# Kernel tuning notes

Hardware: AMD Instinct MI355X
Metric: run time of the kernel (lower is better)

Reference implementation:

```python
import jax, jax.numpy as jnp
import numpy as np

EPS = 1e-8

def l2norm(x, axis):
    # matches torch: x / (sqrt(sum(x^2)) + eps)
    return x / (jnp.sqrt(jnp.sum(x * x, axis=axis, keepdims=True)) + EPS)

def setup_inputs() -> dict:
    key = jax.random.key(0)
    kq, kc, kwq, kbq, kwk, kbk = jax.random.split(key, 6)
    B, QL, SL, D = 128, 512, 1024, 1024
    query = jax.random.normal(kq, (B, QL, D), dtype=jnp.float32)
    context = jax.random.normal(kc, (B, SL, D), dtype=jnp.float32)
    s = 1.0 / np.sqrt(D)
    Wq = jax.random.uniform(kwq, (D, D), jnp.float32, -s, s)
    bq = jax.random.uniform(kbq, (D,), jnp.float32, -s, s)
    Wk = jax.random.uniform(kwk, (D, D), jnp.float32, -s, s)
    bk = jax.random.uniform(kbk, (D,), jnp.float32, -s, s)
    return {"query": query, "context": context, "Wq": Wq, "bq": bq,
            "Wk": Wk, "bk": bk, "smooth": 9.0}

def reference(query, context, Wq, bq, Wk, bk, smooth):
    # linear projections (nn.Linear: x @ W^T + b)
    sim_k = jnp.einsum('bsd,ed->bse', context, Wk) + bk   # (B, SL, D)
    sim_q = jnp.einsum('bqd,ed->bqe', query, Wq) + bq     # (B, QL, D)
    # scores: bmm(sim_k, sim_q^T) -> (B, SL, QL)
    attn = jnp.einsum('bse,bqe->bsq', sim_k, sim_q)
    attn = jnp.where(attn >= 0, attn, 0.1 * attn)          # LeakyReLU(0.1)
    attn = l2norm(attn, axis=2)                            # over queryL dim
    # transpose -> (B, QL, SL), scale, softmax over sourceL
    attn = jax.nn.softmax(attn.transpose(0, 2, 1) * smooth, axis=2)
    # weighted sum of raw context (sim_v = context; fcv unused in original)
    wc = jnp.einsum('bqs,bsd->bqd', attn, context)         # (B, QL, D)
    return l2norm(wc, axis=-1)
```

## Files before the change

### kernel.cpp

```cpp
#include <hip/hip_runtime.h>
#include <hip/hip_bf16.h>

typedef __attribute__((ext_vector_type(8))) short bf16x8;
typedef __attribute__((ext_vector_type(4))) float f32x4;
typedef __attribute__((ext_vector_type(4))) unsigned short u16x4;
typedef __attribute__((ext_vector_type(8))) unsigned short u16x8;

#define DEVINL static __device__ __forceinline__

DEVINL unsigned short f2bf(float f) {
  union { float f; unsigned u; } a; a.f = f;
  return (unsigned short)((a.u + 0x7fffu + ((a.u >> 16) & 1u)) >> 16);
}
DEVINL float bf2f(unsigned short s) {
  union { unsigned u; float f; } a; a.u = ((unsigned)s) << 16; return a.f;
}

typedef __attribute__((address_space(1))) const unsigned char ga_u8;
typedef __attribute__((address_space(3))) unsigned char ls_u8;

constexpr int KD = 1024;
constexpr int NKT = KD / 64;


#define STAGE(b_, mat_, kt_) do { \
    const unsigned short* src_ = (mat_) == 0 ? Az : Bz; \
    const int br_ = (mat_) == 0 ? m0 : n0; \
    char* dst_ = lds + (b_) * 65536 + (mat_) * 32768; \
    _Pragma("unroll") \
    for (int i_ = 0; i_ < 4; ++i_) { \
      const unsigned short* g_ = src_ + (size_t)(br_ + i_ * 64 + sr) * KD + (kt_) * 64 + gc * 8; \
      __builtin_amdgcn_global_load_lds((ga_u8*)g_, (ls_u8*)(dst_ + (i_ * 512 + wv * 64) * 16), 16, 0, 0); \
    } \
  } while (0)

#define KSUB(b_, ks_, STG) do { \
    const char* pA_ = lds + (b_) * 65536; \
    const char* pB_ = pA_ + 32768; \
    const int co_ = (((ks_) * 4 + kg) ^ (ml & 7)) << 4; \
    bf16x8 af_[8], bf_[4]; \
    _Pragma("unroll") \
    for (int mi = 0; mi < 8; ++mi) \
      af_[mi] = *(const bf16x8*)(pA_ + (wm * 128 + mi * 16 + ml) * 128 + co_); \
    _Pragma("unroll") \
    for (int ni = 0; ni < 4; ++ni) \
      bf_[ni] = *(const bf16x8*)(pB_ + (wn * 64 + ni * 16 + ml) * 128 + co_); \
    STG; \
    __builtin_amdgcn_s_setprio(1); \
    _Pragma("unroll") \
    for (int mi = 0; mi < 8; ++mi) \
    _Pragma("unroll") \
    for (int ni = 0; ni < 4; ++ni) \
      acc[mi][ni] = __builtin_amdgcn_mfma_f32_16x16x32_bf16(af_[mi], bf_[ni], acc[mi][ni], 0, 0, 0); \
    __builtin_amdgcn_s_setprio(0); \
  } while (0)

template<int MODE>
__global__ __launch_bounds__(512, 2) void gemm8(
    const unsigned short* __restrict__ A, const unsigned short* __restrict__ B,
    const float* __restrict__ bias, void* __restrict__ Cv,
    float* __restrict__ rnorm2, int mtiles,
    long long sAz, long long sBz, long long sCz, long long sRz, long long sBiasz)
{
  alignas(16) __shared__ char lds[131072];

  const int tid = threadIdx.x;
  const int lane = tid & 63;
  const int wv = tid >> 6;
  const int wm = wv >> 2;
  const int wn = wv & 3;
  const int kg = lane >> 4;
  const int ml = lane & 15;

  const int nwg = (int)gridDim.x;
  const int bid = (int)blockIdx.x;
  const int w = (bid & 7) * (nwg >> 3) + (bid >> 3);
  const int bpz = mtiles * 4;
  const int z = w / bpz;
  const int rem = w - z * bpz;
  const int mt = rem >> 2, nt = rem & 3;
  const int m0 = mt * 256, n0 = nt * 256;

  const unsigned short* Az = A + (size_t)z * (size_t)sAz;
  const unsigned short* Bz = B + (size_t)z * (size_t)sBz;

  const int sr = tid >> 3;
  const int gc = (tid & 7) ^ (sr & 7);

  f32x4 acc[8][4];
  const f32x4 zero4 = {0.f, 0.f, 0.f, 0.f};
#pragma unroll
  for (int i = 0; i < 8; ++i)
#pragma unroll
    for (int j = 0; j < 4; ++j) acc[i][j] = zero4;

  STAGE(0, 0, 0);
  STAGE(0, 1, 0);
  asm volatile("s_waitcnt vmcnt(0)" ::: "memory");
  __builtin_amdgcn_s_barrier();

  for (int t = 0; t < NKT; ++t) {
    const int cur = t & 1;
    const int nxt = cur ^ 1;
    if (t + 1 < NKT) {
      KSUB(cur, 0, STAGE(nxt, 0, t + 1));
      KSUB(cur, 1, STAGE(nxt, 1, t + 1));
    } else {
      KSUB(cur, 0, );
      KSUB(cur, 1, );
    }
    asm volatile("s_waitcnt vmcnt(0)" ::: "memory");
    __builtin_amdgcn_s_barrier();
  }

  float* ew = (float*)(lds + wv * 4352);
  const int erow = lane >> 3;
  const int ec8 = (lane & 7) * 8;
  const int ncol0 = n0 + wn * 64;

  if (MODE == 1) {
    const float* cb = bias + (size_t)z * (size_t)sBiasz;
    f32x4 cb4[8];
#pragma unroll
    for (int mi = 0; mi < 8; ++mi)
      cb4[mi] = *(const f32x4*)(cb + m0 + wm * 128 + mi * 16 + kg * 4);
    float* rn = rnorm2 + (size_t)z * (size_t)sRz;
#pragma unroll
    for (int ni = 0; ni < 4; ++ni) {
      float cs = 0.f;
#pragma unroll
      for (int mi = 0; mi < 8; ++mi)
#pragma unroll
        for (int j = 0; j < 4; ++j) {
          float v = acc[mi][ni][j] + cb4[mi][j];
          v = v >= 0.f ? v : 0.1f * v;
          acc[mi][ni][j] = v;
          cs += v * v;
        }
      cs += __shfl_xor(cs, 16);
      cs += __shfl_xor(cs, 32);
      if (kg == 0) atomicAdd(&rn[ncol0 + ni * 16 + ml], cs);
    }
  }

  f32x4 bv0 = zero4, bv1 = zero4;
  if (MODE == 0) {
    bv0 = *(const f32x4*)(bias + ncol0 + ec8);
    bv1 = *(const f32x4*)(bias + ncol0 + ec8 + 4);
  }

#pragma unroll
  for (int mi = 0; mi < 8; ++mi) {
#pragma unroll
    for (int ni = 0; ni < 4; ++ni)
#pragma unroll
      for (int j = 0; j < 4; ++j)
        ew[(kg * 4 + j) * 68 + ni * 16 + ml] = acc[mi][ni][j];
    const int rb = m0 + wm * 128 + mi * 16;
#pragma unroll
    for (int i = 0; i < 2; ++i) {
      const int r = erow + 8 * i;
      f32x4 x = *(const f32x4*)(&ew[r * 68 + ec8]);
      f32x4 y = *(const f32x4*)(&ew[r * 68 + ec8 + 4]);
      if (MODE == 0 || MODE == 3) {
        unsigned short* C = (unsigned short*)Cv + (size_t)z * (size_t)sCz;
        union { unsigned short s[8]; u16x8 v; } u;
        u.s[0]=f2bf(x[0]+bv0[0]); u.s[1]=f2bf(x[1]+bv0[1]);
        u.s[2]=f2bf(x[2]+bv0[2]); u.s[3]=f2bf(x[3]+bv0[3]);
        u.s[4]=f2bf(y[0]+bv1[0]); u.s[5]=f2bf(y[1]+bv1[1]);
        u.s[6]=f2bf(y[2]+bv1[2]); u.s[7]=f2bf(y[3]+bv1[3]);
        *(u16x8*)(C + (size_t)(rb + r) * 1024 + ncol0 + ec8) = u.v;
      } else {
        float* C = (float*)Cv + (size_t)z * (size_t)sCz;
        *(f32x4*)(C + (size_t)(rb + r) * 1024 + ncol0 + ec8) = x;
        *(f32x4*)(C + (size_t)(rb + r) * 1024 + ncol0 + ec8 + 4) = y;
      }
    }
  }
}

__global__ __launch_bounds__(256) void cvt_bf16_k(
    const float* __restrict__ src, unsigned short* __restrict__ dst)
{
  size_t i = ((size_t)blockIdx.x * 256 + threadIdx.x) * 8;
  f32x4 x = *(const f32x4*)(src + i);
  f32x4 y = *(const f32x4*)(src + i + 4);
  union { unsigned short s[8]; u16x8 v; } u;
  u.s[0]=f2bf(x[0]); u.s[1]=f2bf(x[1]); u.s[2]=f2bf(x[2]); u.s[3]=f2bf(x[3]);
  u.s[4]=f2bf(y[0]); u.s[5]=f2bf(y[1]); u.s[6]=f2bf(y[2]); u.s[7]=f2bf(y[3]);
  *(u16x8*)(dst + i) = u.v;
}

__global__ __launch_bounds__(256) void wT_k(
    const float* __restrict__ W, unsigned short* __restrict__ WT)
{
  __shared__ float tile[32][36];
  const int t = threadIdx.x;
  const int e0 = blockIdx.x * 32, d0 = blockIdx.y * 32;
  const int r = t >> 3, c4 = (t & 7) * 4;
  f32x4 v = *(const f32x4*)(W + (size_t)(e0 + r) * 1024 + d0 + c4);
  *(f32x4*)(&tile[r][c4]) = v;
  __syncthreads();
  u16x4 o;
  o[0] = f2bf(tile[c4 + 0][r]); o[1] = f2bf(tile[c4 + 1][r]);
  o[2] = f2bf(tile[c4 + 2][r]); o[3] = f2bf(tile[c4 + 3][r]);
  *(u16x4*)(WT + (size_t)(d0 + r) * 1024 + e0 + c4) = o;
}

__global__ __launch_bounds__(256) void convert_ctx_k(
    const float* __restrict__ src, unsigned short* __restrict__ dstT,
    unsigned short* __restrict__ dstR)
{
  __shared__ float tile[32][36];
  const int t = threadIdx.x;
  const int s0 = blockIdx.x * 32, d0 = blockIdx.y * 32;
  const float* S = src + (size_t)blockIdx.z * 1048576;
  unsigned short* DT = dstT + (size_t)blockIdx.z * 1048576;
  unsigned short* DR = dstR + (size_t)blockIdx.z * 1048576;
  const int s = t >> 3, d4 = (t & 7) * 4;
  f32x4 v = *(const f32x4*)(S + (size_t)(s0 + s) * 1024 + d0 + d4);
  u16x4 r;
  r[0] = f2bf(v[0]); r[1] = f2bf(v[1]); r[2] = f2bf(v[2]); r[3] = f2bf(v[3]);
  *(u16x4*)(DR + (size_t)(s0 + s) * 1024 + d0 + d4) = r;
  *(f32x4*)(&tile[s][d4]) = v;
  __syncthreads();
  const int d = t >> 3, s4 = (t & 7) * 4;
  u16x4 o;
  o[0] = f2bf(tile[s4 + 0][d]); o[1] = f2bf(tile[s4 + 1][d]);
  o[2] = f2bf(tile[s4 + 2][d]); o[3] = f2bf(tile[s4 + 3][d]);
  *(u16x4*)(DT + (size_t)(d0 + d) * 1024 + s0 + s4) = o;
}

__global__ __launch_bounds__(256) void rowdot_k(
    const unsigned short* __restrict__ Mbf, const float* __restrict__ vec,
    float* __restrict__ outv)
{
  __shared__ float shs[4];
  const int t = threadIdx.x;
  const unsigned short* row = Mbf + (size_t)blockIdx.x * 1024;
  u16x4 a = *(const u16x4*)(row + t * 4);
  f32x4 b = *(const f32x4*)(vec + t * 4);
  float d = bf2f(a[0]) * b[0] + bf2f(a[1]) * b[1] +
            bf2f(a[2]) * b[2] + bf2f(a[3]) * b[3];
#pragma unroll
  for (int o = 32; o; o >>= 1) d += __shfl_xor(d, o);
  if ((t & 63) == 0) shs[t >> 6] = d;
  __syncthreads();
  if (t == 0) outv[blockIdx.x] = shs[0] + shs[1] + shs[2] + shs[3];
}

__global__ __launch_bounds__(256) void cdot_k(
    const unsigned short* __restrict__ qbf, const float* __restrict__ vb,
    const float* __restrict__ bq, const float* __restrict__ bk,
    float* __restrict__ cq)
{
  __shared__ float shs[4];
  const int t = threadIdx.x;
  const unsigned short* row = qbf + (size_t)blockIdx.x * 1024;
  u16x4 a = *(const u16x4*)(row + t * 4);
  f32x4 b = *(const f32x4*)(vb + t * 4);
  f32x4 p = *(const f32x4*)(bq + t * 4);
  f32x4 k = *(const f32x4*)(bk + t * 4);
  float d = bf2f(a[0]) * b[0] + bf2f(a[1]) * b[1] +
            bf2f(a[2]) * b[2] + bf2f(a[3]) * b[3] +
            p[0] * k[0] + p[1] * k[1] + p[2] * k[2] + p[3] * k[3];
#pragma unroll
  for (int o = 32; o; o >>= 1) d += __shfl_xor(d, o);
  if ((t & 63) == 0) shs[t >> 6] = d;
  __syncthreads();
  if (t == 0) cq[blockIdx.x] = shs[0] + shs[1] + shs[2] + shs[3];
}

__global__ __launch_bounds__(256) void softmax_k(
    const float* __restrict__ S, const float* __restrict__ rnorm2,
    const float* __restrict__ smoothp, unsigned short* __restrict__ P)
{
  __shared__ float shm[4], shs[4];
  const int t = threadIdx.x;
  const int z = blockIdx.x >> 9;
  const float sm = *smoothp;
  f32x4 s4 = ((const f32x4*)(S + (size_t)blockIdx.x * 1024))[t];
  f32x4 r4 = ((const f32x4*)(rnorm2 + (size_t)z * 1024))[t];
  f32x4 lg;
  lg[0] = sm * s4[0] / (sqrtf(r4[0]) + 1e-8f);
  lg[1] = sm * s4[1] / (sqrtf(r4[1]) + 1e-8f);
  lg[2] = sm * s4[2] / (sqrtf(r4[2]) + 1e-8f);
  lg[3] = sm * s4[3] / (sqrtf(r4[3]) + 1e-8f);
  float mx = fmaxf(fmaxf(lg[0], lg[1]), fmaxf(lg[2], lg[3]));
#pragma unroll
  for (int o = 32; o; o >>= 1) mx = fmaxf(mx, __shfl_xor(mx, o));
  if ((t & 63) == 0) shm[t >> 6] = mx;
  __syncthreads();
  mx = fmaxf(fmaxf(shm[0], shm[1]), fmaxf(shm[2], shm[3]));
  f32x4 e;
  e[0] = __expf(lg[0] - mx); e[1] = __expf(lg[1] - mx);
  e[2] = __expf(lg[2] - mx); e[3] = __expf(lg[3] - mx);
  float sum = e[0] + e[1] + e[2] + e[3];
#pragma unroll
  for (int o = 32; o; o >>= 1) sum += __shfl_xor(sum, o);
  if ((t & 63) == 0) shs[t >> 6] = sum;
  __syncthreads();
  sum = shs[0] + shs[1] + shs[2] + shs[3];
  float inv = 1.f / sum;
  u16x4 p;
  p[0] = f2bf(e[0] * inv); p[1] = f2bf(e[1] * inv);
  p[2] = f2bf(e[2] * inv); p[3] = f2bf(e[3] * inv);
  ((u16x4*)(P + (size_t)blockIdx.x * 1024))[t] = p;
}

__global__ __launch_bounds__(256) void l2norm_k(
    const float* __restrict__ W, float* __restrict__ O)
{
  __shared__ float shs[4];
  const int t = threadIdx.x;
  f32x4 v = ((const f32x4*)(W + (size_t)blockIdx.x * 1024))[t];
  float ss = v[0]*v[0] + v[1]*v[1] + v[2]*v[2] + v[3]*v[3];
#pragma unroll
  for (int o = 32; o; o >>= 1) ss += __shfl_xor(ss, o);
  if ((t & 63) == 0) shs[t >> 6] = ss;
  __syncthreads();
  ss = shs[0] + shs[1] + shs[2] + shs[3];
  float inv = 1.f / (sqrtf(ss) + 1e-8f);
  f32x4 o4 = { v[0]*inv, v[1]*inv, v[2]*inv, v[3]*inv };
  ((f32x4*)(O + (size_t)blockIdx.x * 1024))[t] = o4;
}

extern "C" void kernel_launch(void* const* d_in, const int* in_sizes, int n_in,
                              void* d_out, int out_size, void* d_ws, size_t ws_size,
                              hipStream_t stream)
{
  (void)in_sizes; (void)n_in; (void)out_size;
  const float* query   = (const float*)d_in[0];
  const float* context = (const float*)d_in[1];
  const float* Wq = (const float*)d_in[2];
  const float* bq = (const float*)d_in[3];
  const float* Wk = (const float*)d_in[4];
  const float* bk = (const float*)d_in[5];
  const float* smooth = (const float*)d_in[6];
  float* out = (float*)d_out;

  const int B = 128, QL = 512, SL = 1024, D = 1024;

  const size_t perB =
      (size_t)QL * D * 2 + (size_t)SL * D * 2 + (size_t)D * SL * 2 +
      (size_t)QL * D * 2 + (size_t)QL * SL * 4 +
      (size_t)SL * 4 + (size_t)QL * 4 + 4096;
  const size_t fixed = 3 * (size_t)D * D * 2 + 2 * (size_t)D * 4 + 16384;
  size_t usable = ws_size > fixed ? ws_size - fixed : 0;
  int C = (int)(usable / perB);
  if (C > B) C = B;
  if (C < 1) C = 1;

  char* p = (char*)d_ws;
  auto alloc = [&](size_t bytes) {
    char* r = p; p += (bytes + 255) & ~(size_t)255; return r;
  };
  unsigned short* wqT  = (unsigned short*)alloc((size_t)D * D * 2);
  unsigned short* wkT  = (unsigned short*)alloc((size_t)D * D * 2);
  unsigned short* WuT  = (unsigned short*)alloc((size_t)D * D * 2);
  float* cu = (float*)alloc((size_t)D * 4);
  float* vb = (float*)alloc((size_t)D * 4);
  unsigned short* qbf  = (unsigned short*)alloc((size_t)C * QL * D * 2);
  unsigned short* ctxbf= (unsigned short*)alloc((size_t)C * SL * D * 2);
  unsigned short* ctxT = (unsigned short*)alloc((size_t)C * D * SL * 2);
  unsigned short* ubf  = (unsigned short*)alloc((size_t)C * QL * D * 2);
  float* Sbuf = (float*)alloc((size_t)C * QL * SL * 4);
  float* rn   = (float*)alloc((size_t)C * SL * 4);
  float* cq   = (float*)alloc((size_t)C * QL * 4);

  wT_k<<<dim3(32, 32), 256, 0, stream>>>(Wq, wqT);
  wT_k<<<dim3(32, 32), 256, 0, stream>>>(Wk, wkT);
  rowdot_k<<<dim3(D), 256, 0, stream>>>(wkT, bq, cu);
  rowdot_k<<<dim3(D), 256, 0, stream>>>(wqT, bk, vb);
  gemm8<3><<<dim3(16), 512, 0, stream>>>(
      wkT, wqT, nullptr, WuT, nullptr, 4, 0, 0, 0, 0, 0);

  for (int b0 = 0; b0 < B; b0 += C) {
    const int Cc = (B - b0) < C ? (B - b0) : C;
    hipMemsetAsync(rn, 0, (size_t)Cc * SL * 4, stream);
    cvt_bf16_k<<<dim3(Cc * QL * D / 2048), 256, 0, stream>>>(
        query + (size_t)b0 * QL * D, qbf);
    convert_ctx_k<<<dim3(32, 32, Cc), 256, 0, stream>>>(
        context + (size_t)b0 * SL * D, ctxT, ctxbf);
    gemm8<0><<<dim3(Cc * 8), 512, 0, stream>>>(
        qbf, WuT, cu, ubf, nullptr, 2,
        (long long)QL * D, 0, (long long)QL * D, 0, 0);
    cdot_k<<<dim3(Cc * QL), 256, 0, stream>>>(qbf, vb, bq, bk, cq);
    gemm8<1><<<dim3(Cc * 8), 512, 0, stream>>>(
        ubf, ctxbf, cq, Sbuf, rn, 2,
        (long long)QL * D, (long long)SL * D, (long long)QL * SL,
        (long long)SL, (long long)QL);
    softmax_k<<<Cc * QL, 256, 0, stream>>>(Sbuf, rn, smooth, ubf );
    gemm8<2><<<dim3(Cc * 8), 512, 0, stream>>>(
        ubf , ctxT, nullptr, Sbuf , nullptr, 2,
        (long long)QL * SL, (long long)D * SL, (long long)QL * D, 0, 0);
    l2norm_k<<<Cc * QL, 256, 0, stream>>>(Sbuf, out + (size_t)b0 * QL * D);
  }
}
```

Measured before the change: 1.045 ms.

## Fuse query conversion with bias dot and compute output row norms in GEMM epilogue

Merges the query bf16 conversion with the per-row bias-correction dot product into one kernel that reads fp32 query once. The final GEMM now writes bf16 output and accumulates per-row sums of squares via atomics, so the l2norm pass reads half the bytes and skips its reduction. It also issues both A and B tile stages in the first k-subtile instead of splitting them across the two subtiles. Costs are an extra rounding of the pre-norm output to bf16, and atomic traffic plus changed load/compute overlap in the GEMM mainloop.

```diff
diff --git a/kernel.cpp b/kernel.cpp
--- a/kernel.cpp
+++ b/kernel.cpp
@@ -33,6 +33,8 @@
       __builtin_amdgcn_global_load_lds((ga_u8*)g_, (ls_u8*)(dst_ + (i_ * 512 + wv * 64) * 16), 16, 0, 0); \
     } \
   } while (0)
+
+#define STAGE2(b_, kt_) do { STAGE(b_, 0, kt_); STAGE(b_, 1, kt_); } while (0)
 
 #define KSUB(b_, ks_, STG) do { \
     const char* pA_ = lds + (b_) * 65536; \
@@ -94,8 +96,7 @@
 #pragma unroll
     for (int j = 0; j < 4; ++j) acc[i][j] = zero4;
 
-  STAGE(0, 0, 0);
-  STAGE(0, 1, 0);
+  STAGE2(0, 0);
   asm volatile("s_waitcnt vmcnt(0)" ::: "memory");
   __builtin_amdgcn_s_barrier();
 
@@ -103,8 +104,8 @@
     const int cur = t & 1;
     const int nxt = cur ^ 1;
     if (t + 1 < NKT) {
-      KSUB(cur, 0, STAGE(nxt, 0, t + 1));
-      KSUB(cur, 1, STAGE(nxt, 1, t + 1));
+      KSUB(cur, 0, STAGE2(nxt, t + 1));
+      KSUB(cur, 1, );
     } else {
       KSUB(cur, 0, );
       KSUB(cur, 1, );
@@ -149,6 +150,8 @@
     bv1 = *(const f32x4*)(bias + ncol0 + ec8 + 4);
   }
 
+  float* rsq = (MODE == 4) ? rnorm2 + (size_t)z * (size_t)sRz : nullptr;
+
 #pragma unroll
   for (int mi = 0; mi < 8; ++mi) {
 #pragma unroll
@@ -162,7 +165,15 @@
       const int r = erow + 8 * i;
       f32x4 x = *(const f32x4*)(&ew[r * 68 + ec8]);
       f32x4 y = *(const f32x4*)(&ew[r * 68 + ec8 + 4]);
-      if (MODE == 0 || MODE == 3) {
+      if (MODE == 4) {
+        float ss = x[0]*x[0] + x[1]*x[1] + x[2]*x[2] + x[3]*x[3] +
+                   y[0]*y[0] + y[1]*y[1] + y[2]*y[2] + y[3]*y[3];
+        ss += __shfl_xor(ss, 1);
+        ss += __shfl_xor(ss, 2);
+        ss += __shfl_xor(ss, 4);
+        if ((lane & 7) == 0) atomicAdd(&rsq[rb + r], ss);
+      }
+      if (MODE == 0 || MODE == 3 || MODE == 4) {
         unsigned short* C = (unsigned short*)Cv + (size_t)z * (size_t)sCz;
         union { unsigned short s[8]; u16x8 v; } u;
         u.s[0]=f2bf(x[0]+bv0[0]); u.s[1]=f2bf(x[1]+bv0[1]);
@@ -179,18 +190,6 @@
   }
 }
 
-__global__ __launch_bounds__(256) void cvt_bf16_k(
-    const float* __restrict__ src, unsigned short* __restrict__ dst)
-{
-  size_t i = ((size_t)blockIdx.x * 256 + threadIdx.x) * 8;
-  f32x4 x = *(const f32x4*)(src + i);
-  f32x4 y = *(const f32x4*)(src + i + 4);
-  union { unsigned short s[8]; u16x8 v; } u;
-  u.s[0]=f2bf(x[0]); u.s[1]=f2bf(x[1]); u.s[2]=f2bf(x[2]); u.s[3]=f2bf(x[3]);
-  u.s[4]=f2bf(y[0]); u.s[5]=f2bf(y[1]); u.s[6]=f2bf(y[2]); u.s[7]=f2bf(y[3]);
-  *(u16x8*)(dst + i) = u.v;
-}
-
 __global__ __launch_bounds__(256) void wT_k(
     const float* __restrict__ W, unsigned short* __restrict__ WT)
 {
@@ -249,26 +248,45 @@
   if (t == 0) outv[blockIdx.x] = shs[0] + shs[1] + shs[2] + shs[3];
 }
 
-__global__ __launch_bounds__(256) void cdot_k(
-    const unsigned short* __restrict__ qbf, const float* __restrict__ vb,
-    const float* __restrict__ bq, const float* __restrict__ bk,
-    float* __restrict__ cq)
+__global__ __launch_bounds__(256) void dot1_k(
+    const float* __restrict__ a, const float* __restrict__ b,
+    float* __restrict__ outv)
 {
   __shared__ float shs[4];
   const int t = threadIdx.x;
-  const unsigned short* row = qbf + (size_t)blockIdx.x * 1024;
-  u16x4 a = *(const u16x4*)(row + t * 4);
-  f32x4 b = *(const f32x4*)(vb + t * 4);
-  f32x4 p = *(const f32x4*)(bq + t * 4);
-  f32x4 k = *(const f32x4*)(bk + t * 4);
-  float d = bf2f(a[0]) * b[0] + bf2f(a[1]) * b[1] +
-            bf2f(a[2]) * b[2] + bf2f(a[3]) * b[3] +
-            p[0] * k[0] + p[1] * k[1] + p[2] * k[2] + p[3] * k[3];
+  f32x4 x = ((const f32x4*)a)[t];
+  f32x4 y = ((const f32x4*)b)[t];
+  float d = x[0]*y[0] + x[1]*y[1] + x[2]*y[2] + x[3]*y[3];
 #pragma unroll
   for (int o = 32; o; o >>= 1) d += __shfl_xor(d, o);
   if ((t & 63) == 0) shs[t >> 6] = d;
   __syncthreads();
-  if (t == 0) cq[blockIdx.x] = shs[0] + shs[1] + shs[2] + shs[3];
+  if (t == 0) outv[0] = shs[0] + shs[1] + shs[2] + shs[3];
+}
+
+__global__ __launch_bounds__(128) void cvtq_dot_k(
+    const float* __restrict__ q, const float* __restrict__ vb,
+    const float* __restrict__ bqbk, unsigned short* __restrict__ qbf,
+    float* __restrict__ cq)
+{
+  __shared__ float sh[2];
+  const int t = threadIdx.x;
+  const size_t base = (size_t)blockIdx.x * 1024 + t * 8;
+  f32x4 x = *(const f32x4*)(q + base);
+  f32x4 y = *(const f32x4*)(q + base + 4);
+  f32x4 v0 = *(const f32x4*)(vb + t * 8);
+  f32x4 v1 = *(const f32x4*)(vb + t * 8 + 4);
+  union { unsigned short s[8]; u16x8 v; } u;
+  u.s[0]=f2bf(x[0]); u.s[1]=f2bf(x[1]); u.s[2]=f2bf(x[2]); u.s[3]=f2bf(x[3]);
+  u.s[4]=f2bf(y[0]); u.s[5]=f2bf(y[1]); u.s[6]=f2bf(y[2]); u.s[7]=f2bf(y[3]);
+  *(u16x8*)(qbf + base) = u.v;
+  float d = x[0]*v0[0] + x[1]*v0[1] + x[2]*v0[2] + x[3]*v0[3] +
+            y[0]*v1[0] + y[1]*v1[1] + y[2]*v1[2] + y[3]*v1[3];
+#pragma unroll
+  for (int o = 32; o; o >>= 1) d += __shfl_xor(d, o);
+  if ((t & 63) == 0) sh[t >> 6] = d;
+  __syncthreads();
+  if (t == 0) cq[blockIdx.x] = sh[0] + sh[1] + bqbk[0];
 }
 
 __global__ __launch_bounds__(256) void softmax_k(
@@ -308,21 +326,17 @@
   ((u16x4*)(P + (size_t)blockIdx.x * 1024))[t] = p;
 }
 
-__global__ __launch_bounds__(256) void l2norm_k(
-    const float* __restrict__ W, float* __restrict__ O)
-{
-  __shared__ float shs[4];
-  const int t = threadIdx.x;
-  f32x4 v = ((const f32x4*)(W + (size_t)blockIdx.x * 1024))[t];
-  float ss = v[0]*v[0] + v[1]*v[1] + v[2]*v[2] + v[3]*v[3];
-#pragma unroll
-  for (int o = 32; o; o >>= 1) ss += __shfl_xor(ss, o);
-  if ((t & 63) == 0) shs[t >> 6] = ss;
-  __syncthreads();
-  ss = shs[0] + shs[1] + shs[2] + shs[3];
-  float inv = 1.f / (sqrtf(ss) + 1e-8f);
-  f32x4 o4 = { v[0]*inv, v[1]*inv, v[2]*inv, v[3]*inv };
-  ((f32x4*)(O + (size_t)blockIdx.x * 1024))[t] = o4;
+__global__ __launch_bounds__(256) void l2fin_k(
+    const unsigned short* __restrict__ Wb, const float* __restrict__ rssq,
+    float* __restrict__ O)
+{
+  const int t = threadIdx.x;
+  const size_t base = (size_t)blockIdx.x * 1024 + t * 4;
+  u16x4 w = *(const u16x4*)(Wb + base);
+  float inv = 1.f / (sqrtf(rssq[blockIdx.x]) + 1e-8f);
+  f32x4 o = { bf2f(w[0]) * inv, bf2f(w[1]) * inv,
+              bf2f(w[2]) * inv, bf2f(w[3]) * inv };
+  *(f32x4*)(O + base) = o;
 }
 
 extern "C" void kernel_launch(void* const* d_in, const int* in_sizes, int n_in,
@@ -344,7 +358,7 @@
   const size_t perB =
       (size_t)QL * D * 2 + (size_t)SL * D * 2 + (size_t)D * SL * 2 +
       (size_t)QL * D * 2 + (size_t)QL * SL * 4 +
-      (size_t)SL * 4 + (size_t)QL * 4 + 4096;
+      (size_t)SL * 4 + (size_t)QL * 4 + (size_t)QL * 4 + 4096;
   const size_t fixed = 3 * (size_t)D * D * 2 + 2 * (size_t)D * 4 + 16384;
   size_t usable = ws_size > fixed ? ws_size - fixed : 0;
   int C = (int)(usable / perB);
@@ -358,8 +372,9 @@
   unsigned short* wqT  = (unsigned short*)alloc((size_t)D * D * 2);
   unsigned short* wkT  = (unsigned short*)alloc((size_t)D * D * 2);
   unsigned short* WuT  = (unsigned short*)alloc((size_t)D * D * 2);
-  float* cu = (float*)alloc((size_t)D * 4);
-  float* vb = (float*)alloc((size_t)D * 4);
+  float* cu   = (float*)alloc((size_t)D * 4);
+  float* vb   = (float*)alloc((size_t)D * 4);
+  float* bqbk = (float*)alloc(256);
   unsigned short* qbf  = (unsigned short*)alloc((size_t)C * QL * D * 2);
   unsigned short* ctxbf= (unsigned short*)alloc((size_t)C * SL * D * 2);
   unsigned short* ctxT = (unsigned short*)alloc((size_t)C * D * SL * 2);
@@ -367,33 +382,37 @@
   float* Sbuf = (float*)alloc((size_t)C * QL * SL * 4);
   float* rn   = (float*)alloc((size_t)C * SL * 4);
   float* cq   = (float*)alloc((size_t)C * QL * 4);
+  float* rsq  = (float*)alloc((size_t)C * QL * 4);
 
   wT_k<<<dim3(32, 32), 256, 0, stream>>>(Wq, wqT);
   wT_k<<<dim3(32, 32), 256, 0, stream>>>(Wk, wkT);
   rowdot_k<<<dim3(D), 256, 0, stream>>>(wkT, bq, cu);
   rowdot_k<<<dim3(D), 256, 0, stream>>>(wqT, bk, vb);
+  dot1_k<<<dim3(1), 256, 0, stream>>>(bq, bk, bqbk);
   gemm8<3><<<dim3(16), 512, 0, stream>>>(
       wkT, wqT, nullptr, WuT, nullptr, 4, 0, 0, 0, 0, 0);
 
   for (int b0 = 0; b0 < B; b0 += C) {
     const int Cc = (B - b0) < C ? (B - b0) : C;
     hipMemsetAsync(rn, 0, (size_t)Cc * SL * 4, stream);
-    cvt_bf16_k<<<dim3(Cc * QL * D / 2048), 256, 0, stream>>>(
-        query + (size_t)b0 * QL * D, qbf);
+    hipMemsetAsync(rsq, 0, (size_t)Cc * QL * 4, stream);
+    cvtq_dot_k<<<dim3(Cc * QL), 128, 0, stream>>>(
+        query + (size_t)b0 * QL * D, vb, bqbk, qbf, cq);
     convert_ctx_k<<<dim3(32, 32, Cc), 256, 0, stream>>>(
         context + (size_t)b0 * SL * D, ctxT, ctxbf);
     gemm8<0><<<dim3(Cc * 8), 512, 0, stream>>>(
         qbf, WuT, cu, ubf, nullptr, 2,
         (long long)QL * D, 0, (long long)QL * D, 0, 0);
-    cdot_k<<<dim3(Cc * QL), 256, 0, stream>>>(qbf, vb, bq, bk, cq);
     gemm8<1><<<dim3(Cc * 8), 512, 0, stream>>>(
         ubf, ctxbf, cq, Sbuf, rn, 2,
         (long long)QL * D, (long long)SL * D, (long long)QL * SL,
         (long long)SL, (long long)QL);
     softmax_k<<<Cc * QL, 256, 0, stream>>>(Sbuf, rn, smooth, ubf );
-    gemm8<2><<<dim3(Cc * 8), 512, 0, stream>>>(
-        ubf , ctxT, nullptr, Sbuf , nullptr, 2,
-        (long long)QL * SL, (long long)D * SL, (long long)QL * D, 0, 0);
-    l2norm_k<<<Cc * QL, 256, 0, stream>>>(Sbuf, out + (size_t)b0 * QL * D);
+    gemm8<4><<<dim3(Cc * 8), 512, 0, stream>>>(
+        ubf , ctxT, nullptr, (unsigned short*)Sbuf , rsq, 2,
+        (long long)QL * SL, (long long)D * SL, (long long)QL * D,
+        (long long)QL, 0);
+    l2fin_k<<<dim3(Cc * QL), 256, 0, stream>>>(
+        (const unsigned short*)Sbuf, rsq, out + (size_t)b0 * QL * D);
   }
 }
```

Measured after the change: 991.8 us. -5.1%, faster.
